# Performance work log

Hardware: AMD Instinct MI355X
Metric: run time of the kernel (lower is better)

The kernel has to match this reference:

```python
import jax, jax.numpy as jnp
import numpy as np

BS, D = 4096, 768

def setup_inputs() -> dict:
    key = jax.random.key(0)
    k1, k2 = jax.random.split(key)
    code_vec = jax.random.normal(k1, (BS, D), dtype=jnp.float32)
    nl_vec = jax.random.normal(k2, (BS, D), dtype=jnp.float32)
    return {"code_vec": code_vec, "nl_vec": nl_vec, "bs": BS}

def reference(code_vec, nl_vec, bs):
    # scores[i, j] = <nl_vec[i], code_vec[j]>  -- expressed as a GEMM
    scores = jnp.einsum("nd,md->nm", nl_vec, code_vec)  # [bs, bs]
    # CrossEntropyLoss with labels = arange(bs): mean of -log_softmax diagonal
    logprobs = jax.nn.log_softmax(scores, axis=-1)
    labels = jnp.arange(bs)
    loss = -jnp.mean(logprobs[labels, labels])
    return loss
```

## Files before the change

kernel.cpp:

```cpp
#include <hip/hip_runtime.h>
#include <hip/hip_bf16.h>
#include <math.h>

#define BSZ 4096
#define DIM 768
#define BK 64
#define NTILE (DIM / BK)
#define CSPLIT 16

typedef __attribute__((ext_vector_type(8))) short short8;
typedef __attribute__((ext_vector_type(4))) float f32x4;

__device__ __forceinline__ unsigned short f2bf(float f) {
  unsigned u = __float_as_uint(f);
  u += 0x7fffu + ((u >> 16) & 1u);
  return (unsigned short)(u >> 16);
}

__device__ __forceinline__ void gload16(const void* gp, const void* lp) {
  __builtin_amdgcn_global_load_lds(
      (const __attribute__((address_space(1))) unsigned int*)(size_t)gp,
      (__attribute__((address_space(3))) unsigned int*)(unsigned int)(size_t)lp,
      16, 0, 0);
}

__device__ __forceinline__ short8 lds_ld(const unsigned char* p) {
  return *(const short8*)p;
}

__global__ void convert_kernel(const float* __restrict__ src0,
                               const float* __restrict__ src1,
                               unsigned short* __restrict__ dst0,
                               unsigned short* __restrict__ dst1)
{
  const int n4 = (BSZ * DIM) / 4;
  int i = blockIdx.x * blockDim.x + threadIdx.x;
  const float* src;
  unsigned short* dst;
  if (i < n4) { src = src0; dst = dst0; }
  else        { src = src1; dst = dst1; i -= n4; }
  float4 v = *reinterpret_cast<const float4*>(src + (size_t)i * 4);
  ushort4 o;
  o.x = f2bf(v.x); o.y = f2bf(v.y); o.z = f2bf(v.z); o.w = f2bf(v.w);
  *reinterpret_cast<ushort4*>(dst + (size_t)i * 4) = o;
}

__global__ __launch_bounds__(512, 2)
void gemm_lse_kernel(const unsigned short* __restrict__ A,
                     const unsigned short* __restrict__ B,
                     float* __restrict__ pm, float* __restrict__ ps,
                     float* __restrict__ diag)
{
  __shared__ alignas(16) unsigned char smem[131072];
  const int tid  = threadIdx.x;
  const int w    = tid >> 6;
  const int lane = tid & 63;
  const int lr   = lane & 15;
  const int hi   = lane >> 4;
  const int wm   = w >> 2;
  const int wn   = w & 3;
  const int i0 = blockIdx.x << 8;
  const int j0 = blockIdx.y << 8;

  const int fb0 = (hi ^ (lr & 7)) << 4;
  const int fb1 = ((4 + hi) ^ (lr & 7)) << 4;
  const int arowb = (wm * 128 + lr) * 128;
  const int browb = (wn * 64 + lr) * 128;

  const int srow = tid >> 3;
  const int gcol = ((tid & 7) ^ (srow & 7)) << 3;
  const unsigned short* pA = A + (size_t)(i0 + srow) * DIM + gcol;
  const unsigned short* pB = B + (size_t)(j0 + srow) * DIM + gcol;
  const int ldsbase = w << 10;

  f32x4 acc[8][4];
#pragma unroll
  for (int m = 0; m < 8; ++m)
#pragma unroll
    for (int n = 0; n < 4; ++n)
      acc[m][n] = (f32x4){0.f, 0.f, 0.f, 0.f};

#pragma unroll
  for (int q = 0; q < 4; ++q) {
    gload16(pA + (size_t)(q * 64) * DIM, smem + q * 8192 + ldsbase);
    gload16(pB + (size_t)(q * 64) * DIM, smem + 65536 + q * 8192 + ldsbase);
  }
  asm volatile("s_waitcnt vmcnt(0)" ::: "memory");
  __builtin_amdgcn_s_barrier();

#pragma unroll 2
  for (int u = 0; u < NTILE; ++u) {
    const int c = u & 1;
    const unsigned char* la = smem + c * 32768;
    const unsigned char* lb = smem + 65536 + c * 32768;
    unsigned char* na = smem + (c ^ 1) * 32768;
    unsigned char* nb = smem + 65536 + (c ^ 1) * 32768;
    const bool st = (u + 1 < NTILE);
    const size_t kn = (size_t)(u + 1) * BK;

    short8 aF[4], bF[4];

#pragma unroll
    for (int n = 0; n < 4; ++n) bF[n] = lds_ld(lb + browb + n * 2048 + fb0);
#pragma unroll
    for (int m = 0; m < 4; ++m) aF[m] = lds_ld(la + arowb + m * 2048 + fb0);
    if (st) {
      gload16(pA + kn,                  na + ldsbase);
      gload16(pA + (size_t)64 * DIM + kn,  na + 8192 + ldsbase);
      gload16(pB + kn,                  nb + ldsbase);
      gload16(pB + (size_t)64 * DIM + kn,  nb + 8192 + ldsbase);
    }
    __builtin_amdgcn_s_barrier();
    asm volatile("s_waitcnt lgkmcnt(0)" ::: "memory");
    __builtin_amdgcn_s_setprio(1);
#pragma unroll
    for (int m = 0; m < 4; ++m)
#pragma unroll
      for (int n = 0; n < 4; ++n)
        acc[m][n] = __builtin_amdgcn_mfma_f32_16x16x32_bf16(aF[m], bF[n], acc[m][n], 0, 0, 0);
    __builtin_amdgcn_s_setprio(0);
    __builtin_amdgcn_s_barrier();

#pragma unroll
    for (int m = 0; m < 4; ++m) aF[m] = lds_ld(la + arowb + (4 + m) * 2048 + fb0);
    if (st) {
      gload16(pA + (size_t)128 * DIM + kn, na + 2 * 8192 + ldsbase);
      gload16(pA + (size_t)192 * DIM + kn, na + 3 * 8192 + ldsbase);
      gload16(pB + (size_t)128 * DIM + kn, nb + 2 * 8192 + ldsbase);
      gload16(pB + (size_t)192 * DIM + kn, nb + 3 * 8192 + ldsbase);
    }
    __builtin_amdgcn_s_barrier();
    asm volatile("s_waitcnt lgkmcnt(0)" ::: "memory");
    __builtin_amdgcn_s_setprio(1);
#pragma unroll
    for (int m = 0; m < 4; ++m)
#pragma unroll
      for (int n = 0; n < 4; ++n)
        acc[4 + m][n] = __builtin_amdgcn_mfma_f32_16x16x32_bf16(aF[m], bF[n], acc[4 + m][n], 0, 0, 0);
    __builtin_amdgcn_s_setprio(0);
    __builtin_amdgcn_s_barrier();

#pragma unroll
    for (int n = 0; n < 4; ++n) bF[n] = lds_ld(lb + browb + n * 2048 + fb1);
#pragma unroll
    for (int m = 0; m < 4; ++m) aF[m] = lds_ld(la + arowb + m * 2048 + fb1);
    __builtin_amdgcn_s_barrier();
    asm volatile("s_waitcnt lgkmcnt(0)" ::: "memory");
    __builtin_amdgcn_s_setprio(1);
#pragma unroll
    for (int m = 0; m < 4; ++m)
#pragma unroll
      for (int n = 0; n < 4; ++n)
        acc[m][n] = __builtin_amdgcn_mfma_f32_16x16x32_bf16(aF[m], bF[n], acc[m][n], 0, 0, 0);
    __builtin_amdgcn_s_setprio(0);
    __builtin_amdgcn_s_barrier();

#pragma unroll
    for (int m = 0; m < 4; ++m) aF[m] = lds_ld(la + arowb + (4 + m) * 2048 + fb1);
    __builtin_amdgcn_s_barrier();
    asm volatile("s_waitcnt lgkmcnt(0)" ::: "memory");
    __builtin_amdgcn_s_setprio(1);
#pragma unroll
    for (int m = 0; m < 4; ++m)
#pragma unroll
      for (int n = 0; n < 4; ++n)
        acc[4 + m][n] = __builtin_amdgcn_mfma_f32_16x16x32_bf16(aF[m], bF[n], acc[4 + m][n], 0, 0, 0);
    __builtin_amdgcn_s_setprio(0);
    asm volatile("s_waitcnt vmcnt(0)" ::: "memory");
    __builtin_amdgcn_s_barrier();
  }

  __syncthreads();

  if (i0 == j0) {
#pragma unroll
    for (int m = 0; m < 8; ++m)
#pragma unroll
      for (int n = 0; n < 4; ++n)
#pragma unroll
        for (int rr = 0; rr < 4; ++rr) {
          const int rl = wm * 128 + m * 16 + (hi << 2) + rr;
          const int cl = wn * 64 + n * 16 + lr;
          if (rl == cl) diag[i0 + rl] = acc[m][n][rr];
        }
  }

  float* redm = (float*)smem;
  float* reds = (float*)(smem + 4096);

#pragma unroll
  for (int m = 0; m < 8; ++m) {
    float mx[4], sm[4];
#pragma unroll
    for (int rr = 0; rr < 4; ++rr) {
      float v = fmaxf(fmaxf(acc[m][0][rr], acc[m][1][rr]),
                      fmaxf(acc[m][2][rr], acc[m][3][rr]));
      mx[rr] = v;
    }
#pragma unroll
    for (int sh = 1; sh < 16; sh <<= 1)
#pragma unroll
      for (int rr = 0; rr < 4; ++rr)
        mx[rr] = fmaxf(mx[rr], __shfl_xor(mx[rr], sh, 64));
#pragma unroll
    for (int rr = 0; rr < 4; ++rr) {
      float s = 0.f;
#pragma unroll
      for (int n = 0; n < 4; ++n) s += __expf(acc[m][n][rr] - mx[rr]);
      sm[rr] = s;
    }
#pragma unroll
    for (int sh = 1; sh < 16; sh <<= 1)
#pragma unroll
      for (int rr = 0; rr < 4; ++rr)
        sm[rr] += __shfl_xor(sm[rr], sh, 64);
    if (lr == 0) {
#pragma unroll
      for (int rr = 0; rr < 4; ++rr) {
        const int rl = wm * 128 + m * 16 + (hi << 2) + rr;
        redm[(wn << 8) + rl] = mx[rr];
        reds[(wn << 8) + rl] = sm[rr];
      }
    }
  }
  __syncthreads();

  if (tid < 256) {
    float m = redm[tid];
#pragma unroll
    for (int v = 1; v < 4; ++v) m = fmaxf(m, redm[(v << 8) + tid]);
    float s = 0.f;
#pragma unroll
    for (int v = 0; v < 4; ++v) s += reds[(v << 8) + tid] * __expf(redm[(v << 8) + tid] - m);
    pm[(size_t)blockIdx.y * BSZ + i0 + tid] = m;
    ps[(size_t)blockIdx.y * BSZ + i0 + tid] = s;
  }
}

__global__ void combine1_kernel(const float* __restrict__ pm, const float* __restrict__ ps,
                                const float* __restrict__ diag, float* __restrict__ partial)
{
  __shared__ float red[256];
  const int row = blockIdx.x * 256 + threadIdx.x;
  float m = -INFINITY;
#pragma unroll
  for (int c = 0; c < CSPLIT; ++c) m = fmaxf(m, pm[(size_t)c * BSZ + row]);
  float s = 0.f;
#pragma unroll
  for (int c = 0; c < CSPLIT; ++c) s += ps[(size_t)c * BSZ + row] * __expf(pm[(size_t)c * BSZ + row] - m);
  red[threadIdx.x] = (m + __logf(s)) - diag[row];
  __syncthreads();
  for (int off = 128; off > 0; off >>= 1) {
    if (threadIdx.x < off) red[threadIdx.x] += red[threadIdx.x + off];
    __syncthreads();
  }
  if (threadIdx.x == 0) partial[blockIdx.x] = red[0];
}

__global__ void combine2_kernel(const float* __restrict__ partial, float* __restrict__ out)
{
  if (threadIdx.x == 0) {
    float s = 0.f;
    for (int i = 0; i < 16; ++i) s += partial[i];
    out[0] = s / (float)BSZ;
  }
}

extern "C" void kernel_launch(void* const* d_in, const int* in_sizes, int n_in,
                              void* d_out, int out_size, void* d_ws, size_t ws_size,
                              hipStream_t stream) {
  const float* code = (const float*)d_in[0];
  const float* nl   = (const float*)d_in[1];
  float* out = (float*)d_out;

  char* ws = (char*)d_ws;
  unsigned short* Abf = (unsigned short*)ws;
  unsigned short* Bbf = (unsigned short*)(ws + (size_t)BSZ * DIM * 2);
  float* pm   = (float*)(ws + (size_t)BSZ * DIM * 4);
  float* ps   = pm + (size_t)CSPLIT * BSZ;
  float* diag = ps + (size_t)CSPLIT * BSZ;
  float* partial = diag + BSZ;

  const int n4 = (BSZ * DIM) / 4;
  convert_kernel<<<(2 * n4) / 256, 256, 0, stream>>>(nl, code, Abf, Bbf);

  dim3 grid(BSZ / 256, BSZ / 256);
  gemm_lse_kernel<<<grid, 512, 0, stream>>>(Abf, Bbf, pm, ps, diag);

  combine1_kernel<<<BSZ / 256, 256, 0, stream>>>(pm, ps, diag, partial);
  combine2_kernel<<<1, 64, 0, stream>>>(partial, out);
}
```

Before: 46.55 us.

## Fuse LSE combine stages into GEMM kernel via last-block atomic counters

Removes the two separate combine kernel launches and moves their work into the tail of the GEMM kernel. Per-row-block atomic counters, zeroed by the convert kernel, let the last column block of each row group do the cross-split log-sum-exp merge. A second counter lets the last finishing group sum the partials into the scalar loss. This saves two launch gaps at the cost of threadfences and atomics in every GEMM block, and a serialized tail in the last finishers.

After: 78.59 us. 68.8% more time.

```diff
diff --git a/kernel.cpp b/kernel.cpp
--- a/kernel.cpp
+++ b/kernel.cpp
@@ -31,8 +31,10 @@
 __global__ void convert_kernel(const float* __restrict__ src0,
                                const float* __restrict__ src1,
                                unsigned short* __restrict__ dst0,
-                               unsigned short* __restrict__ dst1)
+                               unsigned short* __restrict__ dst1,
+                               unsigned int* __restrict__ cnt)
 {
+  if (blockIdx.x == 0 && threadIdx.x <= CSPLIT) cnt[threadIdx.x] = 0u;
   const int n4 = (BSZ * DIM) / 4;
   int i = blockIdx.x * blockDim.x + threadIdx.x;
   const float* src;
@@ -49,7 +51,10 @@
 void gemm_lse_kernel(const unsigned short* __restrict__ A,
                      const unsigned short* __restrict__ B,
                      float* __restrict__ pm, float* __restrict__ ps,
-                     float* __restrict__ diag)
+                     float* __restrict__ diag,
+                     float* __restrict__ partial,
+                     unsigned int* __restrict__ cnt,
+                     float* __restrict__ out)
 {
   __shared__ alignas(16) unsigned char smem[131072];
   const int tid  = threadIdx.x;
@@ -235,34 +240,44 @@
     pm[(size_t)blockIdx.y * BSZ + i0 + tid] = m;
     ps[(size_t)blockIdx.y * BSZ + i0 + tid] = s;
   }
-}
-
-__global__ void combine1_kernel(const float* __restrict__ pm, const float* __restrict__ ps,
-                                const float* __restrict__ diag, float* __restrict__ partial)
-{
-  __shared__ float red[256];
-  const int row = blockIdx.x * 256 + threadIdx.x;
-  float m = -INFINITY;
-#pragma unroll
-  for (int c = 0; c < CSPLIT; ++c) m = fmaxf(m, pm[(size_t)c * BSZ + row]);
-  float s = 0.f;
-#pragma unroll
-  for (int c = 0; c < CSPLIT; ++c) s += ps[(size_t)c * BSZ + row] * __expf(pm[(size_t)c * BSZ + row] - m);
-  red[threadIdx.x] = (m + __logf(s)) - diag[row];
+
+  __threadfence();
   __syncthreads();
-  for (int off = 128; off > 0; off >>= 1) {
-    if (threadIdx.x < off) red[threadIdx.x] += red[threadIdx.x + off];
+  __shared__ unsigned int sord;
+  if (tid == 0) sord = atomicAdd(&cnt[blockIdx.x], 1u);
+  __syncthreads();
+  if (sord == CSPLIT - 1) {
+    __threadfence();
+    float val = 0.f;
+    if (tid < 256) {
+      const int row = i0 + tid;
+      float m = -INFINITY;
+#pragma unroll
+      for (int c = 0; c < CSPLIT; ++c) m = fmaxf(m, pm[(size_t)c * BSZ + row]);
+      float s = 0.f;
+#pragma unroll
+      for (int c = 0; c < CSPLIT; ++c)
+        s += ps[(size_t)c * BSZ + row] * __expf(pm[(size_t)c * BSZ + row] - m);
+      val = (m + __logf(s)) - diag[row];
+    }
+    float* red2 = (float*)smem;
+    red2[tid] = val;
     __syncthreads();
-  }
-  if (threadIdx.x == 0) partial[blockIdx.x] = red[0];
-}
-
-__global__ void combine2_kernel(const float* __restrict__ partial, float* __restrict__ out)
-{
-  if (threadIdx.x == 0) {
-    float s = 0.f;
-    for (int i = 0; i < 16; ++i) s += partial[i];
-    out[0] = s / (float)BSZ;
+    for (int off = 256; off > 0; off >>= 1) {
+      if (tid < off) red2[tid] += red2[tid + off];
+      __syncthreads();
+    }
+    if (tid == 0) {
+      partial[blockIdx.x] = red2[0];
+      __threadfence();
+      unsigned int d = atomicAdd(&cnt[CSPLIT], 1u);
+      if (d == CSPLIT - 1) {
+        __threadfence();
+        float s = 0.f;
+        for (int i = 0; i < CSPLIT; ++i) s += partial[i];
+        out[0] = s / (float)BSZ;
+      }
+    }
   }
 }
 
@@ -280,13 +295,11 @@
   float* ps   = pm + (size_t)CSPLIT * BSZ;
   float* diag = ps + (size_t)CSPLIT * BSZ;
   float* partial = diag + BSZ;
+  unsigned int* cnt = (unsigned int*)(partial + CSPLIT);
 
   const int n4 = (BSZ * DIM) / 4;
-  convert_kernel<<<(2 * n4) / 256, 256, 0, stream>>>(nl, code, Abf, Bbf);
+  convert_kernel<<<(2 * n4) / 256, 256, 0, stream>>>(nl, code, Abf, Bbf, cnt);
 
   dim3 grid(BSZ / 256, BSZ / 256);
-  gemm_lse_kernel<<<grid, 512, 0, stream>>>(Abf, Bbf, pm, ps, diag);
-
-  combine1_kernel<<<BSZ / 256, 256, 0, stream>>>(pm, ps, diag, partial);
-  combine2_kernel<<<1, 64, 0, stream>>>(partial, out);
-}
+  gemm_lse_kernel<<<grid, 512, 0, stream>>>(Abf, Bbf, pm, ps, diag, partial, cnt, out);
+}
```
